# Performance work log

Hardware: AMD Instinct MI355X
Metric: run time of the kernel (lower is better)

The kernel has to match this reference:

```python
import jax, jax.numpy as jnp
import numpy as np

EMBED = 512
HEADS = 8
HIDDEN = 4 * EMBED
EPS = 1e-5


def setup_inputs() -> dict:
    key = jax.random.key(0)
    ks = jax.random.split(key, 12)
    s = lambda fan_in: 1.0 / np.sqrt(fan_in)
    return {
        "x": jax.random.normal(ks[0], (4, 2048, EMBED), dtype=jnp.float32),
        "ln1_g": jnp.ones((EMBED,), jnp.float32),
        "ln1_b": jnp.zeros((EMBED,), jnp.float32),
        "qkv_w": jax.random.uniform(ks[1], (EMBED, 3 * EMBED), jnp.float32, -s(EMBED), s(EMBED)),
        "qkv_b": jax.random.uniform(ks[2], (3 * EMBED,), jnp.float32, -s(EMBED), s(EMBED)),
        "proj_w": jax.random.uniform(ks[3], (EMBED, EMBED), jnp.float32, -s(EMBED), s(EMBED)),
        "proj_b": jax.random.uniform(ks[4], (EMBED,), jnp.float32, -s(EMBED), s(EMBED)),
        "ln2_g": jnp.ones((EMBED,), jnp.float32),
        "ln2_b": jnp.zeros((EMBED,), jnp.float32),
        "fc1_w": jax.random.uniform(ks[5], (EMBED, HIDDEN), jnp.float32, -s(EMBED), s(EMBED)),
        "fc1_b": jax.random.uniform(ks[6], (HIDDEN,), jnp.float32, -s(EMBED), s(EMBED)),
        "fc2_w": jax.random.uniform(ks[7], (HIDDEN, EMBED), jnp.float32, -s(HIDDEN), s(HIDDEN)),
        "fc2_b": jax.random.uniform(ks[8], (EMBED,), jnp.float32, -s(HIDDEN), s(HIDDEN)),
    }


def _layernorm(x, g, b):
    mu = jnp.mean(x, axis=-1, keepdims=True)
    var = jnp.mean(jnp.square(x - mu), axis=-1, keepdims=True)
    return (x - mu) * jax.lax.rsqrt(var + EPS) * g + b


def reference(x, ln1_g, ln1_b, qkv_w, qkv_b, proj_w, proj_b,
              ln2_g, ln2_b, fc1_w, fc1_b, fc2_w, fc2_b):
    B, N, C = x.shape
    H, D = HEADS, C // HEADS
    scale = D ** -0.5

    # --- attention sub-block (pre-LN) ---
    h = _layernorm(x, ln1_g, ln1_b)
    qkv = h @ qkv_w + qkv_b                      # [B,N,3C]
    q, k, v = jnp.split(qkv, 3, axis=-1)
    q = q.reshape(B, N, H, D).transpose(0, 2, 1, 3)  # [B,H,N,D]
    k = k.reshape(B, N, H, D).transpose(0, 2, 1, 3)
    v = v.reshape(B, N, H, D).transpose(0, 2, 1, 3)
    attn = jnp.einsum('bhqd,bhkd->bhqk', q, k) * scale
    attn = jax.nn.softmax(attn, axis=-1)
    o = jnp.einsum('bhqk,bhkd->bhqd', attn, v)
    o = o.transpose(0, 2, 1, 3).reshape(B, N, C)
    x = x + (o @ proj_w + proj_b)

    # --- MLP sub-block (pre-LN, exact GELU) ---
    h = _layernorm(x, ln2_g, ln2_b)
    h = jax.nn.gelu(h @ fc1_w + fc1_b, approximate=False)
    x = x + (h @ fc2_w + fc2_b)
    return x
```

## Files before the change

### kernel.cpp

```cpp
#include <hip/hip_runtime.h>
#include <math.h>


using bf16x8 = __attribute__((ext_vector_type(8))) short;
using f32x4  = __attribute__((ext_vector_type(4))) float;
using f32x16 = __attribute__((ext_vector_type(16))) float;

typedef unsigned short u16;
typedef unsigned int   u32;

__device__ __forceinline__ u16 f2bf(float f) {
    u32 u; __builtin_memcpy(&u, &f, 4);
    u32 r = u + 0x7FFFu + ((u >> 16) & 1u);
    return (u16)(r >> 16);
}
__device__ __forceinline__ u32 fbits(float f) {
    u32 u; __builtin_memcpy(&u, &f, 4); return u;
}
__device__ __forceinline__ float f_from_bits(u32 u) {
    float f; __builtin_memcpy(&f, &u, 4); return f;
}
__device__ __forceinline__ u32 pack_trunc(float lo, float hi) {
    return __builtin_amdgcn_perm(fbits(hi), fbits(lo), 0x07060302u);
}
__device__ __forceinline__ void gload16(const void* g, void* l) {
    __builtin_amdgcn_global_load_lds(
        (const __attribute__((address_space(1))) unsigned int*)g,
        (__attribute__((address_space(3))) unsigned int*)l, 16, 0, 0);
}

__global__ __launch_bounds__(256) void k_pre(
        const float* __restrict__ w0, u16* __restrict__ d0,
        const float* __restrict__ w1, u16* __restrict__ d1,
        const float* __restrict__ w2, u16* __restrict__ d2,
        const float* __restrict__ w3, u16* __restrict__ d3,
        const float* __restrict__ x, const float* __restrict__ g,
        const float* __restrict__ bta, u16* __restrict__ hout) {
    __shared__ float tile[32][33];
    const int bid = blockIdx.x;
    if (bid < 3072) {
        const float* w; u16* dst; int K, N, tb;
        if (bid < 768)       { w = w0; dst = d0; K = 512;  N = 1536; tb = bid; }
        else if (bid < 1024) { w = w1; dst = d1; K = 512;  N = 512;  tb = bid - 768; }
        else if (bid < 2048) { w = w2; dst = d2; K = 512;  N = 2048; tb = bid - 1024; }
        else                 { w = w3; dst = d3; K = 2048; N = 512;  tb = bid - 2048; }
        const int nb = N >> 5;
        const int k0 = (tb / nb) << 5;
        const int n0 = (tb % nb) << 5;
        const int c = threadIdx.x & 31, r = threadIdx.x >> 5;
#pragma unroll
        for (int i = 0; i < 4; i++)
            tile[r + i * 8][c] = w[(size_t)(k0 + r + i * 8) * N + n0 + c];
        __syncthreads();
#pragma unroll
        for (int i = 0; i < 4; i++)
            dst[(size_t)(n0 + r + i * 8) * K + k0 + c] = f2bf(tile[c][r + i * 8]);
    } else {
        const int row  = ((bid - 3072) << 2) + (threadIdx.x >> 6);
        const int lane = threadIdx.x & 63;
        const float* xr = x + (size_t)row * 512 + lane * 8;
        float4 a = *(const float4*)xr;
        float4 c = *(const float4*)(xr + 4);
        float s = a.x + a.y + a.z + a.w + c.x + c.y + c.z + c.w;
        float q = a.x*a.x + a.y*a.y + a.z*a.z + a.w*a.w
                + c.x*c.x + c.y*c.y + c.z*c.z + c.w*c.w;
#pragma unroll
        for (int off = 32; off; off >>= 1) {
            s += __shfl_xor(s, off, 64);
            q += __shfl_xor(q, off, 64);
        }
        const float mean = s * (1.0f / 512.0f);
        const float var  = q * (1.0f / 512.0f) - mean * mean;
        const float rstd = rsqrtf(var + 1e-5f);
        float vv[8] = {a.x, a.y, a.z, a.w, c.x, c.y, c.z, c.w};
#pragma unroll
        for (int j = 0; j < 8; j++) {
            const int col = lane * 8 + j;
            hout[(size_t)row * 512 + col] = f2bf((vv[j] - mean) * rstd * g[col] + bta[col]);
        }
    }
}

__global__ __launch_bounds__(256) void k_ln(const float* __restrict__ x,
                                            const float* __restrict__ g,
                                            const float* __restrict__ bta,
                                            u16* __restrict__ out) {
    const int row  = (blockIdx.x << 2) + (threadIdx.x >> 6);
    const int lane = threadIdx.x & 63;
    const float* xr = x + (size_t)row * 512 + lane * 8;
    float4 a = *(const float4*)xr;
    float4 c = *(const float4*)(xr + 4);
    float s = a.x + a.y + a.z + a.w + c.x + c.y + c.z + c.w;
    float q = a.x*a.x + a.y*a.y + a.z*a.z + a.w*a.w
            + c.x*c.x + c.y*c.y + c.z*c.z + c.w*c.w;
#pragma unroll
    for (int off = 32; off; off >>= 1) {
        s += __shfl_xor(s, off, 64);
        q += __shfl_xor(q, off, 64);
    }
    const float mean = s * (1.0f / 512.0f);
    const float var  = q * (1.0f / 512.0f) - mean * mean;
    const float rstd = rsqrtf(var + 1e-5f);
    float vv[8] = {a.x, a.y, a.z, a.w, c.x, c.y, c.z, c.w};
#pragma unroll
    for (int j = 0; j < 8; j++) {
        const int col = lane * 8 + j;
        out[(size_t)row * 512 + col] = f2bf((vv[j] - mean) * rstd * g[col] + bta[col]);
    }
}

template <int EP, int TN>
__global__ __launch_bounds__(256, 3) void k_gemm(const u16* __restrict__ A,
                                                 const u16* __restrict__ Bt,
                                                 const float* __restrict__ bias,
                                                 const float* __restrict__ res,
                                                 float* __restrict__ outF,
                                                 u16* __restrict__ outB,
                                                 u16* __restrict__ out2,
                                                 int M, int N, int K) {
    constexpr int NT = TN / 32;
    __shared__ u16 As[128 * 64];
    __shared__ u16 Bs[TN * 64];
    const int nb = N / TN;
    const int xg = blockIdx.x & 7, sg = blockIdx.x >> 3;
    const int m0 = ((sg / nb) * 8 + xg) << 7;
    const int n0 = (sg % nb) * TN;
    const int t = threadIdx.x, lane = t & 63, w = t >> 6;
    const int wr = (w >> 1) << 6;
    const int wc = (w & 1) * (TN / 2);
    const int quad = lane >> 4, l15 = lane & 15;
    const int x7 = l15 & 7;

    f32x4 acc[4][NT];
#pragma unroll
    for (int i = 0; i < 4; i++)
#pragma unroll
        for (int j = 0; j < NT; j++) acc[i][j] = (f32x4){0.f, 0.f, 0.f, 0.f};

    const size_t Kb = (size_t)K * 2;
    const char* ga = (const char*)A + (size_t)m0 * Kb;
    const char* gb = (const char*)Bt + (size_t)n0 * Kb;
    const int o0 = t * 16;

    for (int k0 = 0; k0 < K; k0 += 64) {
        const int kb = k0 * 2;
#pragma unroll
        for (int i = 0; i < 4; i++) {
            const int o4 = i * 4096 + o0;
            const int row = o4 >> 7;
            const int lc = ((o4 >> 4) & 7) ^ (row & 7);
            gload16(ga + (size_t)row * Kb + kb + lc * 16, (char*)As + o4);
        }
#pragma unroll
        for (int i = 0; i < TN / 32; i++) {
            const int o4 = i * 4096 + o0;
            const int row = o4 >> 7;
            const int lc = ((o4 >> 4) & 7) ^ (row & 7);
            gload16(gb + (size_t)row * Kb + kb + lc * 16, (char*)Bs + o4);
        }
        __syncthreads();
#pragma unroll
        for (int ks = 0; ks < 2; ks++) {
            const int cidx = ((ks * 4 + quad) ^ x7) * 8;
            bf16x8 af[4], bfr[NT];
#pragma unroll
            for (int i = 0; i < 4; i++)
                af[i] = *(const bf16x8*)(As + (wr + i * 16 + l15) * 64 + cidx);
#pragma unroll
            for (int j = 0; j < NT; j++)
                bfr[j] = *(const bf16x8*)(Bs + (wc + j * 16 + l15) * 64 + cidx);
#pragma unroll
            for (int mt = 0; mt < 4; mt++)
#pragma unroll
                for (int nt = 0; nt < NT; nt++)
                    acc[mt][nt] = __builtin_amdgcn_mfma_f32_16x16x32_bf16(
                        af[mt], bfr[nt], acc[mt][nt], 0, 0, 0);
        }
        __syncthreads();
    }

    const bool vpart = (EP == 3) && (n0 >= 1024);
    const bool qpart = (EP == 3) && (n0 < 512);
#pragma unroll
    for (int mt = 0; mt < 4; mt++)
#pragma unroll
        for (int nt = 0; nt < NT; nt++) {
            const int col = n0 + wc + nt * 16 + l15;
            const float bi = bias[col];
            const int row0 = m0 + wr + mt * 16 + quad * 4;
            if (vpart) {
                const int b = row0 >> 11, key = row0 & 2047;
                const int hd = col - 1024;
                u32 p0 = (u32)f2bf(acc[mt][nt][0] + bi) |
                         ((u32)f2bf(acc[mt][nt][1] + bi) << 16);
                u32 p1 = (u32)f2bf(acc[mt][nt][2] + bi) |
                         ((u32)f2bf(acc[mt][nt][3] + bi) << 16);
                *(uint2*)(out2 + (size_t)(b * 512 + hd) * 2048 + key) = make_uint2(p0, p1);
            } else {
#pragma unroll
                for (int r = 0; r < 4; r++) {
                    const int row = row0 + r;
                    float v = acc[mt][nt][r] + bi;
                    const size_t oi = (size_t)row * N + col;
                    if (EP == 1) {
                        float y = v * (0.79788456f + 0.035677408f * v * v);
                        y = fminf(y, 40.0f);
                        float tE = exp2f(y * 2.88539008f);
                        v = v * tE * __builtin_amdgcn_rcpf(tE + 1.0f);
                    }
                    if (qpart) v *= 0.18033688f;
                    if (EP == 2) outF[oi] = v + res[oi];
                    else         outB[oi] = f2bf(v);
                }
            }
        }
}

__global__ __launch_bounds__(256, 4) void k_attn(const u16* __restrict__ qkv,
                                                 const u16* __restrict__ vt,
                                                 u16* __restrict__ po0,
                                                 u16* __restrict__ po1,
                                                 float* __restrict__ pden) {
    __shared__ u16 smem[16384];
    const int bid = blockIdx.x;
    const int h = bid & 7, sg = bid >> 3;
    const int qt = sg & 15, kh = (sg >> 4) & 1, b = sg >> 5;
    const int q0 = qt << 7;
    const int t = threadIdx.x, lane = t & 63, w = t >> 6;
    const int l31 = lane & 31, hi = lane >> 5;
    const int x7 = l31 & 7;

    char* sb = (char*)smem;
    const char* gk = (const char*)qkv + (size_t)((b << 11) + (kh << 10)) * 3072 + 1024 + h * 128;
    const char* gv = (const char*)vt + (size_t)((b << 3) + h) * 64 * 4096 + (kh << 10) * 2;

#pragma unroll
    for (int i = 0; i < 2; i++) {
        const int o4 = i * 4096 + t * 16;
        const int row = o4 >> 7;
        const int lc = ((o4 >> 4) & 7) ^ (row & 7);
        gload16(gk + (size_t)row * 3072 + lc * 16, sb + o4);
        gload16(gv + (size_t)row * 4096 + lc * 16, sb + 8192 + o4);
    }

    bf16x8 qf[4];
    {
        const u16* gqp = qkv + (size_t)((b << 11) + q0 + w * 32 + l31) * 1536 + h * 64 + hi * 8;
#pragma unroll
        for (int ks = 0; ks < 4; ks++)
            qf[ks] = *(const bf16x8*)(gqp + ks * 16);
    }

    f32x16 accO[2];
#pragma unroll
    for (int i = 0; i < 16; i++) { accO[0][i] = 0.f; accO[1][i] = 0.f; }
    float dn = 0.f;

    for (int kt = 0; kt < 16; kt++) {
        const int cur = kt & 1;
        __syncthreads();
        if (kt < 15) {
            const int kk2 = (kt + 1) << 6;
            char* db = sb + (cur ^ 1) * 16384;
#pragma unroll
            for (int i = 0; i < 2; i++) {
                const int o4 = i * 4096 + t * 16;
                const int row = o4 >> 7;
                const int lc = ((o4 >> 4) & 7) ^ (row & 7);
                gload16(gk + (size_t)(kk2 + row) * 3072 + lc * 16, db + o4);
                gload16(gv + (size_t)row * 4096 + (size_t)kk2 * 2 + lc * 16, db + 8192 + o4);
            }
        }
        const u16* Ksc = smem + cur * 8192;
        const u16* Vsc = Ksc + 4096;

        f32x16 s2[2];
#pragma unroll
        for (int i = 0; i < 16; i++) { s2[0][i] = 0.f; s2[1][i] = 0.f; }
#pragma unroll
        for (int ks = 0; ks < 4; ks++) {
            const int cx = ((ks * 2 + hi) ^ x7) * 8;
            bf16x8 kf0 = *(const bf16x8*)(Ksc + l31 * 64 + cx);
            bf16x8 kf1 = *(const bf16x8*)(Ksc + (32 + l31) * 64 + cx);
            __builtin_amdgcn_s_setprio(1);
            s2[0] = __builtin_amdgcn_mfma_f32_32x32x16_bf16(kf0, qf[ks], s2[0], 0, 0, 0);
            s2[1] = __builtin_amdgcn_mfma_f32_32x32x16_bf16(kf1, qf[ks], s2[1], 0, 0, 0);
            __builtin_amdgcn_s_setprio(0);
        }

        u32 pfu[4][4];
#pragma unroll
        for (int mt = 0; mt < 2; mt++) {
            float pv[16];
#pragma unroll
            for (int r = 0; r < 16; r++) {
                pv[r] = __builtin_amdgcn_exp2f(s2[mt][r]);
                dn += pv[r];
            }
            u32 pk[4][2];
#pragma unroll
            for (int c = 0; c < 4; c++)
#pragma unroll
                for (int m = 0; m < 2; m++)
                    pk[c][m] = pack_trunc(pv[4 * c + 2 * m], pv[4 * c + 2 * m + 1]);
#pragma unroll
            for (int ksl = 0; ksl < 2; ksl++)
#pragma unroll
                for (int m = 0; m < 2; m++) {
                    auto rr = __builtin_amdgcn_permlane32_swap(
                        pk[ksl * 2][m], pk[ksl * 2 + 1][m], false, false);
                    pfu[mt * 2 + ksl][m]     = rr[0];
                    pfu[mt * 2 + ksl][m + 2] = rr[1];
                }
        }
        __builtin_amdgcn_sched_barrier(0);

#pragma unroll
        for (int ks = 0; ks < 4; ks++) {
            u32 pw[4] = {pfu[ks][0], pfu[ks][1], pfu[ks][2], pfu[ks][3]};
            bf16x8 pfv;
            __builtin_memcpy(&pfv, pw, 16);
            const int cx = ((ks * 2 + hi) ^ x7) * 8;
            bf16x8 vf0 = *(const bf16x8*)(Vsc + l31 * 64 + cx);
            bf16x8 vf1 = *(const bf16x8*)(Vsc + (32 + l31) * 64 + cx);
            __builtin_amdgcn_s_setprio(1);
            accO[0] = __builtin_amdgcn_mfma_f32_32x32x16_bf16(vf0, pfv, accO[0], 0, 0, 0);
            accO[1] = __builtin_amdgcn_mfma_f32_32x32x16_bf16(vf1, pfv, accO[1], 0, 0, 0);
            __builtin_amdgcn_s_setprio(0);
        }
    }

    u16* po = kh ? po1 : po0;
    dn += __shfl_xor(dn, 32, 64);
    const int qg = q0 + w * 32 + l31;
    if (hi == 0)
        pden[(size_t)(((kh << 5) + (b << 3) + h) << 11) + qg] = dn;
#pragma unroll
    for (int mtd = 0; mtd < 2; mtd++)
#pragma unroll
        for (int g = 0; g < 4; g++) {
            const u32 p0 = (u32)f2bf(accO[mtd][4 * g + 0]) |
                           ((u32)f2bf(accO[mtd][4 * g + 1]) << 16);
            const u32 p1 = (u32)f2bf(accO[mtd][4 * g + 2]) |
                           ((u32)f2bf(accO[mtd][4 * g + 3]) << 16);
            const int d0 = mtd * 32 + g * 8 + hi * 4;
            *(uint2*)(po + (size_t)((b << 11) + qg) * 512 + h * 64 + d0) =
                make_uint2(p0, p1);
        }
}

__global__ __launch_bounds__(256) void k_combine(u16* __restrict__ po0,
                                                 const u16* __restrict__ po1,
                                                 const float* __restrict__ pden) {
    const int idx8 = (blockIdx.x * 256 + threadIdx.x) * 8;
    const int row = idx8 >> 9, col = idx8 & 511;
    const int h = col >> 6, q = row & 2047, b = row >> 11;
    const size_t di = (size_t)(((b << 3) + h) << 11) + q;
    const float den = pden[di] + pden[di + (32 << 11)];
    const float r = __builtin_amdgcn_rcpf(den);
    uint4 a = *(const uint4*)(po0 + idx8);
    uint4 c = *(const uint4*)(po1 + idx8);
    u32 av[4] = {a.x, a.y, a.z, a.w}, cv[4] = {c.x, c.y, c.z, c.w}, ov[4];
#pragma unroll
    for (int i = 0; i < 4; i++) {
        const float lo = (f_from_bits(av[i] << 16) + f_from_bits(cv[i] << 16)) * r;
        const float hi = (f_from_bits(av[i] & 0xFFFF0000u) +
                          f_from_bits(cv[i] & 0xFFFF0000u)) * r;
        ov[i] = (u32)f2bf(lo) | ((u32)f2bf(hi) << 16);
    }
    *(uint4*)(po0 + idx8) = make_uint4(ov[0], ov[1], ov[2], ov[3]);
}

extern "C" void kernel_launch(void* const* d_in, const int* in_sizes, int n_in,
                              void* d_out, int out_size, void* d_ws, size_t ws_size,
                              hipStream_t stream) {
    const float* x      = (const float*)d_in[0];
    const float* ln1_g  = (const float*)d_in[1];
    const float* ln1_b  = (const float*)d_in[2];
    const float* qkv_w  = (const float*)d_in[3];
    const float* qkv_b  = (const float*)d_in[4];
    const float* proj_w = (const float*)d_in[5];
    const float* proj_b = (const float*)d_in[6];
    const float* ln2_g  = (const float*)d_in[7];
    const float* ln2_b  = (const float*)d_in[8];
    const float* fc1_w  = (const float*)d_in[9];
    const float* fc1_b  = (const float*)d_in[10];
    const float* fc2_w  = (const float*)d_in[11];
    const float* fc2_b  = (const float*)d_in[12];
    float* out = (float*)d_out;
    char* ws = (char*)d_ws;

    u16*   qkv_wT = (u16*)(ws + 0);
    u16*   proj_wT= (u16*)(ws + 1572864);
    u16*   fc1_wT = (u16*)(ws + 2097152);
    u16*   fc2_wT = (u16*)(ws + 4194304);
    u16*   h      = (u16*)(ws + 6291456);
    float* pden   = (float*)(ws + 6291456);
    u16*   qkv    = (u16*)(ws + 14680064);
    u16*   vt     = (u16*)(ws + 39845888);
    u16*   o      = (u16*)(ws + 48234496);
    u16*   po1    = (u16*)(ws + 56623104);
    float* x1     = (float*)(ws + 56623104);
    u16*   f1     = (u16*)(ws + 14680064);
    u16*   h2     = h;

    k_pre<<<5120, 256, 0, stream>>>(qkv_w, qkv_wT, proj_w, proj_wT,
                                    fc1_w, fc1_wT, fc2_w, fc2_wT,
                                    x, ln1_g, ln1_b, h);
    k_gemm<3,128><<<(8192/128)*(1536/128), 256, 0, stream>>>(
        h, qkv_wT, qkv_b, nullptr, nullptr, qkv, vt, 8192, 1536, 512);
    k_attn<<<1024, 256, 0, stream>>>(qkv, vt, o, po1, pden);
    k_combine<<<2048, 256, 0, stream>>>(o, po1, pden);
    k_gemm<2,64><<<(8192/128)*(512/64), 256, 0, stream>>>(
        o, proj_wT, proj_b, x, x1, nullptr, nullptr, 8192, 512, 512);
    k_ln<<<2048, 256, 0, stream>>>(x1, ln2_g, ln2_b, h2);
    k_gemm<1,128><<<(8192/128)*(2048/128), 256, 0, stream>>>(
        h2, fc1_wT, fc1_b, nullptr, nullptr, f1, nullptr, 8192, 2048, 512);
    k_gemm<2,64><<<(8192/128)*(512/64), 256, 0, stream>>>(
        f1, fc2_wT, fc2_b, x1, out, nullptr, nullptr, 8192, 512, 2048);
}
```

Before: 244.0 us.

## Drop split-K attention and combine kernel; normalize output in-kernel

Attention blocks now loop over all 2048 keys instead of splitting the key range across two blocks, so the separate combine kernel, partial-output buffers and denominator buffer go away. The softmax denominator is applied directly before writing bf16 output. This removes one launch and the partial write/read round trip, but halves the grid to 512 blocks, which lowers parallelism and doubles per-block latency. A sched_barrier between the softmax and PV phases is also removed, giving the compiler more freedom in instruction scheduling.

New measurement: 234.3 us. 1.04x faster.

```diff
diff --git a/kernel.cpp b/kernel.cpp
--- a/kernel.cpp
+++ b/kernel.cpp
@@ -218,21 +218,19 @@
 
 __global__ __launch_bounds__(256, 4) void k_attn(const u16* __restrict__ qkv,
                                                  const u16* __restrict__ vt,
-                                                 u16* __restrict__ po0,
-                                                 u16* __restrict__ po1,
-                                                 float* __restrict__ pden) {
+                                                 u16* __restrict__ o) {
     __shared__ u16 smem[16384];
     const int bid = blockIdx.x;
     const int h = bid & 7, sg = bid >> 3;
-    const int qt = sg & 15, kh = (sg >> 4) & 1, b = sg >> 5;
+    const int qt = sg & 15, b = sg >> 4;
     const int q0 = qt << 7;
     const int t = threadIdx.x, lane = t & 63, w = t >> 6;
     const int l31 = lane & 31, hi = lane >> 5;
     const int x7 = l31 & 7;
 
     char* sb = (char*)smem;
-    const char* gk = (const char*)qkv + (size_t)((b << 11) + (kh << 10)) * 3072 + 1024 + h * 128;
-    const char* gv = (const char*)vt + (size_t)((b << 3) + h) * 64 * 4096 + (kh << 10) * 2;
+    const char* gk = (const char*)qkv + (size_t)(b << 11) * 3072 + 1024 + h * 128;
+    const char* gv = (const char*)vt + (size_t)((b << 3) + h) * 64 * 4096;
 
 #pragma unroll
     for (int i = 0; i < 2; i++) {
@@ -256,10 +254,10 @@
     for (int i = 0; i < 16; i++) { accO[0][i] = 0.f; accO[1][i] = 0.f; }
     float dn = 0.f;
 
-    for (int kt = 0; kt < 16; kt++) {
+    for (int kt = 0; kt < 32; kt++) {
         const int cur = kt & 1;
         __syncthreads();
-        if (kt < 15) {
+        if (kt < 31) {
             const int kk2 = (kt + 1) << 6;
             char* db = sb + (cur ^ 1) * 16384;
 #pragma unroll
@@ -313,7 +311,6 @@
                     pfu[mt * 2 + ksl][m + 2] = rr[1];
                 }
         }
-        __builtin_amdgcn_sched_barrier(0);
 
 #pragma unroll
         for (int ks = 0; ks < 4; ks++) {
@@ -330,45 +327,21 @@
         }
     }
 
-    u16* po = kh ? po1 : po0;
     dn += __shfl_xor(dn, 32, 64);
+    const float rdn = __builtin_amdgcn_rcpf(dn);
     const int qg = q0 + w * 32 + l31;
-    if (hi == 0)
-        pden[(size_t)(((kh << 5) + (b << 3) + h) << 11) + qg] = dn;
 #pragma unroll
     for (int mtd = 0; mtd < 2; mtd++)
 #pragma unroll
         for (int g = 0; g < 4; g++) {
-            const u32 p0 = (u32)f2bf(accO[mtd][4 * g + 0]) |
-                           ((u32)f2bf(accO[mtd][4 * g + 1]) << 16);
-            const u32 p1 = (u32)f2bf(accO[mtd][4 * g + 2]) |
-                           ((u32)f2bf(accO[mtd][4 * g + 3]) << 16);
+            const u32 p0 = (u32)f2bf(accO[mtd][4 * g + 0] * rdn) |
+                           ((u32)f2bf(accO[mtd][4 * g + 1] * rdn) << 16);
+            const u32 p1 = (u32)f2bf(accO[mtd][4 * g + 2] * rdn) |
+                           ((u32)f2bf(accO[mtd][4 * g + 3] * rdn) << 16);
             const int d0 = mtd * 32 + g * 8 + hi * 4;
-            *(uint2*)(po + (size_t)((b << 11) + qg) * 512 + h * 64 + d0) =
+            *(uint2*)(o + (size_t)((b << 11) + qg) * 512 + h * 64 + d0) =
                 make_uint2(p0, p1);
         }
-}
-
-__global__ __launch_bounds__(256) void k_combine(u16* __restrict__ po0,
-                                                 const u16* __restrict__ po1,
-                                                 const float* __restrict__ pden) {
-    const int idx8 = (blockIdx.x * 256 + threadIdx.x) * 8;
-    const int row = idx8 >> 9, col = idx8 & 511;
-    const int h = col >> 6, q = row & 2047, b = row >> 11;
-    const size_t di = (size_t)(((b << 3) + h) << 11) + q;
-    const float den = pden[di] + pden[di + (32 << 11)];
-    const float r = __builtin_amdgcn_rcpf(den);
-    uint4 a = *(const uint4*)(po0 + idx8);
-    uint4 c = *(const uint4*)(po1 + idx8);
-    u32 av[4] = {a.x, a.y, a.z, a.w}, cv[4] = {c.x, c.y, c.z, c.w}, ov[4];
-#pragma unroll
-    for (int i = 0; i < 4; i++) {
-        const float lo = (f_from_bits(av[i] << 16) + f_from_bits(cv[i] << 16)) * r;
-        const float hi = (f_from_bits(av[i] & 0xFFFF0000u) +
-                          f_from_bits(cv[i] & 0xFFFF0000u)) * r;
-        ov[i] = (u32)f2bf(lo) | ((u32)f2bf(hi) << 16);
-    }
-    *(uint4*)(po0 + idx8) = make_uint4(ov[0], ov[1], ov[2], ov[3]);
 }
 
 extern "C" void kernel_launch(void* const* d_in, const int* in_sizes, int n_in,
@@ -395,11 +368,9 @@
     u16*   fc1_wT = (u16*)(ws + 2097152);
     u16*   fc2_wT = (u16*)(ws + 4194304);
     u16*   h      = (u16*)(ws + 6291456);
-    float* pden   = (float*)(ws + 6291456);
     u16*   qkv    = (u16*)(ws + 14680064);
     u16*   vt     = (u16*)(ws + 39845888);
     u16*   o      = (u16*)(ws + 48234496);
-    u16*   po1    = (u16*)(ws + 56623104);
     float* x1     = (float*)(ws + 56623104);
     u16*   f1     = (u16*)(ws + 14680064);
     u16*   h2     = h;
@@ -409,8 +380,7 @@
                                     x, ln1_g, ln1_b, h);
     k_gemm<3,128><<<(8192/128)*(1536/128), 256, 0, stream>>>(
         h, qkv_wT, qkv_b, nullptr, nullptr, qkv, vt, 8192, 1536, 512);
-    k_attn<<<1024, 256, 0, stream>>>(qkv, vt, o, po1, pden);
-    k_combine<<<2048, 256, 0, stream>>>(o, po1, pden);
+    k_attn<<<512, 256, 0, stream>>>(qkv, vt, o);
     k_gemm<2,64><<<(8192/128)*(512/64), 256, 0, stream>>>(
         o, proj_wT, proj_b, x, x1, nullptr, nullptr, 8192, 512, 512);
     k_ln<<<2048, 256, 0, stream>>>(x1, ln2_g, ln2_b, h2);
```
